# Kernel tuning notes

Measured on AMD Instinct MI355X. Metric: run time of the kernel, lower is better.

Reference implementation:

```python
import jax, jax.numpy as jnp
import numpy as np

N_NODES = 100000
N_EDGES = 800000
D_IN = 128
HOPS = 2
BN_EPS = 1e-5


def setup_inputs() -> dict:
    key = jax.random.key(0)
    ks = jax.random.split(key, 12)
    d_cat = D_IN * (HOPS + 1)  # 384
    inp = {
        "x": jax.random.normal(ks[0], (N_NODES, D_IN), dtype=jnp.float32),
        "edge_index": jax.random.randint(ks[1], (2, N_EDGES), 0, N_NODES, dtype=jnp.int32),
        "W0": jax.random.normal(ks[2], (HOPS + 1, D_IN, D_IN), dtype=jnp.float32) / np.sqrt(D_IN),
        "b0": jax.random.normal(ks[3], (HOPS + 1, D_IN), dtype=jnp.float32) * 0.01,
        "W1": jax.random.normal(ks[4], (HOPS + 1, d_cat, D_IN), dtype=jnp.float32) / np.sqrt(d_cat),
        "b1": jax.random.normal(ks[5], (HOPS + 1, D_IN), dtype=jnp.float32) * 0.01,
        "W2": jax.random.normal(ks[6], (HOPS + 1, d_cat, D_IN), dtype=jnp.float32) / np.sqrt(d_cat),
        "b2": jax.random.normal(ks[7], (HOPS + 1, D_IN), dtype=jnp.float32) * 0.01,
        "bn_gamma": jnp.ones((2, d_cat), dtype=jnp.float32),
        "bn_beta": jnp.zeros((2, d_cat), dtype=jnp.float32),
    }
    return inp


def _gcn_norm(edge_index, n):
    # gcn_norm(add_self_loops=False): deg over col, w_e = d^-1/2[row]*d^-1/2[col]
    row, col = edge_index[0], edge_index[1]
    deg = jax.ops.segment_sum(jnp.ones(row.shape[0], jnp.float32), col, num_segments=n)
    dinv = jnp.where(deg > 0, jax.lax.rsqrt(jnp.maximum(deg, 1.0)), 0.0)
    w = dinv[row] * dinv[col]
    return row, col, w


def _spmm(row, col, w, xj, n):
    # adj_t = SparseTensor(row=col, col=row, value=w): out[col_e] += w_e * x[row_e]
    return jax.ops.segment_sum(w[:, None] * xj[row], col, num_segments=n)


def _mixhop_layer(x, W, b, row, col, w, n):
    outs = [x @ W[0] + b[0]]
    for j in range(1, HOPS + 1):
        xj = x @ W[j] + b[j]
        for _ in range(j):
            xj = _spmm(row, col, w, xj, n)
        outs.append(xj)
    return jnp.concatenate(outs, axis=1)


def _bn(x, g, b):
    mu = jnp.mean(x, axis=0)
    var = jnp.mean(jnp.square(x - mu), axis=0)
    return (x - mu) * jax.lax.rsqrt(var + BN_EPS) * g + b


def reference(x, edge_index, W0, b0, W1, b1, W2, b2, bn_gamma, bn_beta):
    n = x.shape[0]
    row, col, w = _gcn_norm(edge_index, n)
    h = _mixhop_layer(x, W0, b0, row, col, w, n)
    h = jax.nn.relu(_bn(h, bn_gamma[0], bn_beta[0]))  # dropout: eval mode (identity)
    h = _mixhop_layer(h, W1, b1, row, col, w, n)
    h = jax.nn.relu(_bn(h, bn_gamma[1], bn_beta[1]))
    h = _mixhop_layer(h, W2, b2, row, col, w, n)
    return h
```

## Files before the change

kernel.cpp:

```cpp
#include <hip/hip_runtime.h>
#include <hip/hip_bf16.h>

#define NN 100000
#define NE 800000
#define DIN 128
#define DCAT 384
#define BN_EPS 1e-5

typedef __attribute__((ext_vector_type(8))) short bf16x8;
typedef __attribute__((ext_vector_type(4))) float f32x4;
typedef __attribute__((ext_vector_type(4))) int   i32x4;


__global__ void count_deg_k(const int* __restrict__ ei, int* __restrict__ deg) {
    int i = blockIdx.x * blockDim.x + threadIdx.x;
    if (i < NE) atomicAdd(&deg[ei[NE + i]], 1);
}

__global__ void dinv_k(const int* __restrict__ deg, float* __restrict__ dinv) {
    int i = blockIdx.x * blockDim.x + threadIdx.x;
    if (i < NN) {
        int d = deg[i];
        dinv[i] = (d > 0) ? rsqrtf((float)d) : 0.f;
    }
}

__global__ void scan1_k(const int* __restrict__ deg, int* __restrict__ out,
                        int* __restrict__ bsum) {
    __shared__ int s[1024];
    int i = blockIdx.x * 1024 + threadIdx.x;
    int v = (i < NN) ? deg[i] : 0;
    s[threadIdx.x] = v;
    __syncthreads();
    for (int off = 1; off < 1024; off <<= 1) {
        int t = (threadIdx.x >= off) ? s[threadIdx.x - off] : 0;
        __syncthreads();
        s[threadIdx.x] += t;
        __syncthreads();
    }
    if (i < NN) out[i] = s[threadIdx.x] - v;
    if (threadIdx.x == 1023) bsum[blockIdx.x] = s[1023];
}

__global__ void scan2_k(int* __restrict__ bsum, int nb) {
    if (threadIdx.x == 0) {
        int acc = 0;
        for (int b = 0; b < nb; ++b) { int v = bsum[b]; bsum[b] = acc; acc += v; }
    }
}

__global__ void scan3_k(int* __restrict__ ptr, int* __restrict__ cursor,
                        const int* __restrict__ bsum) {
    int i = blockIdx.x * 1024 + threadIdx.x;
    if (i < NN) {
        int p = ptr[i] + bsum[blockIdx.x];
        ptr[i] = p;
        cursor[i] = p;
    }
    if (i == NN) ptr[NN] = NE;
}

__global__ void scatter_k(const int* __restrict__ ei, const float* __restrict__ dinv,
                          int* __restrict__ cursor, int* __restrict__ crow,
                          float* __restrict__ cw) {
    int i = blockIdx.x * blockDim.x + threadIdx.x;
    if (i >= NE) return;
    int r = ei[i];
    int c = ei[NE + i];
    int p = atomicAdd(&cursor[c], 1);
    crow[p] = r;
    cw[p] = dinv[r] * dinv[c];
}


__device__ inline void split_trunc(float x, short& hi, short& lo) {
    unsigned u = __builtin_bit_cast(unsigned, x);
    hi = (short)(u >> 16);
    float hf = __builtin_bit_cast(float, u & 0xFFFF0000u);
    __hip_bfloat16 l = __float2bfloat16(x - hf);
    lo = *reinterpret_cast<short*>(&l);
}

__global__ void wsplit_k(const float* __restrict__ W, int K,
                         short* __restrict__ Wth, short* __restrict__ Wtl) {
    int i = blockIdx.x * 256 + threadIdx.x;
    if (i >= 3 * K * 128) return;
    int c = i & 127;
    int k = (i >> 7) % K;
    int j = i / (K * 128);
    short h, l;
    split_trunc(W[i], h, l);
    size_t o = (size_t)j * 128 * 384 + (size_t)c * 384 + k;
    Wth[o] = h;
    Wtl[o] = l;
}

__global__ __launch_bounds__(256) void bnsplit_k(
    const float* __restrict__ H, int Kc4,
    const float2* __restrict__ coef, int use_bn,
    short* __restrict__ Xh, short* __restrict__ Xl) {
    size_t n4 = (size_t)NN * Kc4;
    for (size_t i = (size_t)blockIdx.x * blockDim.x + threadIdx.x; i < n4;
         i += (size_t)gridDim.x * blockDim.x) {
        float4 v = ((const float4*)H)[i];
        if (use_bn) {
            int c4 = (int)(i % Kc4) * 4;
            float2 c0 = coef[c4 + 0], c1 = coef[c4 + 1];
            float2 c2 = coef[c4 + 2], c3 = coef[c4 + 3];
            v.x = fmaxf(v.x * c0.x + c0.y, 0.f);
            v.y = fmaxf(v.y * c1.x + c1.y, 0.f);
            v.z = fmaxf(v.z * c2.x + c2.y, 0.f);
            v.w = fmaxf(v.w * c3.x + c3.y, 0.f);
        }
        short h0, l0, h1, l1, h2, l2, h3, l3;
        split_trunc(v.x, h0, l0);
        split_trunc(v.y, h1, l1);
        split_trunc(v.z, h2, l2);
        split_trunc(v.w, h3, l3);
        ((short4*)Xh)[i] = make_short4(h0, h1, h2, h3);
        ((short4*)Xl)[i] = make_short4(l0, l1, l2, l3);
    }
}

#define GPITCH 40

__global__ __launch_bounds__(256, 3) void gemm3m_k(
    const short* __restrict__ Xh, const short* __restrict__ Xl, int K,
    const short* __restrict__ Wth, const short* __restrict__ Wtl,
    const float* __restrict__ bias,
    float* __restrict__ o0, int p0,
    float* __restrict__ o1, int p1,
    float* __restrict__ o2, int p2) {
    __shared__ short Ah[2][128 * GPITCH];
    __shared__ short Al[2][128 * GPITCH];

    const int nwg = gridDim.x;
    const int id  = blockIdx.x;
    const int q = nwg >> 3, r = nwg & 7;
    const int xcd = id & 7, ii = id >> 3;
    const int swz = (xcd < r ? xcd * (q + 1) : r * (q + 1) + (xcd - r) * q) + ii;
    const int j  = swz % 3;
    const int m0 = (swz / 3) * 128;

    const int t    = threadIdx.x;
    const int lane = t & 63;
    const int wv   = t >> 6;
    const int wr   = (wv >> 1) * 64;
    const int wc   = (wv & 1) * 64;
    const int lr   = lane & 15;
    const int lk   = lane >> 4;

    const short* Wh = Wth + (size_t)j * 128 * 384;
    const short* Wl = Wtl + (size_t)j * 128 * 384;

    const int arow = t >> 1;
    const int akc  = (t & 1) * 16;
    int gr = m0 + arow;
    if (gr >= NN) gr = NN - 1;
    const short* pAh = Xh + (size_t)gr * K + akc;
    const short* pAl = Xl + (size_t)gr * K + akc;
    const int soff = arow * GPITCH + akc;

    f32x4 acc[4][4];
#pragma unroll
    for (int a = 0; a < 4; ++a)
#pragma unroll
        for (int b = 0; b < 4; ++b) acc[a][b] = (f32x4){0.f, 0.f, 0.f, 0.f};

    const int NT = K >> 5;

    {
        i32x4 h0 = *(const i32x4*)(pAh);
        i32x4 h1 = *(const i32x4*)(pAh + 8);
        i32x4 l0 = *(const i32x4*)(pAl);
        i32x4 l1 = *(const i32x4*)(pAl + 8);
        *(i32x4*)&Ah[0][soff]     = h0;
        *(i32x4*)&Ah[0][soff + 8] = h1;
        *(i32x4*)&Al[0][soff]     = l0;
        *(i32x4*)&Al[0][soff + 8] = l1;
    }
    __syncthreads();

    int cur = 0;
    for (int tt = 0; tt < NT; ++tt) {
        const int kb = tt << 5;

        bf16x8 bh[4], bl[4];
#pragma unroll
        for (int nc = 0; nc < 4; ++nc) {
            const size_t bo = (size_t)(wc + nc * 16 + lr) * 384 + kb + lk * 8;
            bh[nc] = *(const bf16x8*)(Wh + bo);
            bl[nc] = *(const bf16x8*)(Wl + bo);
        }

        i32x4 h0, h1, l0, l1;
        if (tt + 1 < NT) {
            const int ko = kb + 32;
            h0 = *(const i32x4*)(pAh + ko);
            h1 = *(const i32x4*)(pAh + ko + 8);
            l0 = *(const i32x4*)(pAl + ko);
            l1 = *(const i32x4*)(pAl + ko + 8);
        }

        bf16x8 ah[4], al[4];
#pragma unroll
        for (int mr = 0; mr < 4; ++mr) {
            const int rr = (wr + mr * 16 + lr) * GPITCH + lk * 8;
            ah[mr] = *(const bf16x8*)&Ah[cur][rr];
            al[mr] = *(const bf16x8*)&Al[cur][rr];
        }

#pragma unroll
        for (int nc = 0; nc < 4; ++nc) {
#pragma unroll
            for (int mr = 0; mr < 4; ++mr) {
                f32x4 a = acc[mr][nc];
                a = __builtin_amdgcn_mfma_f32_16x16x32_bf16(al[mr], bh[nc], a, 0, 0, 0);
                a = __builtin_amdgcn_mfma_f32_16x16x32_bf16(ah[mr], bl[nc], a, 0, 0, 0);
                a = __builtin_amdgcn_mfma_f32_16x16x32_bf16(ah[mr], bh[nc], a, 0, 0, 0);
                acc[mr][nc] = a;
            }
        }

        if (tt + 1 < NT) {
            const int nb = cur ^ 1;
            *(i32x4*)&Ah[nb][soff]     = h0;
            *(i32x4*)&Ah[nb][soff + 8] = h1;
            *(i32x4*)&Al[nb][soff]     = l0;
            *(i32x4*)&Al[nb][soff + 8] = l1;
        }
        __syncthreads();
        cur ^= 1;
    }

    float* dst;
    int pitch;
    if (j == 0)      { dst = o0; pitch = p0; }
    else if (j == 1) { dst = o1; pitch = p1; }
    else             { dst = o2; pitch = p2; }

#pragma unroll
    for (int nc = 0; nc < 4; ++nc) {
        int col = wc + nc * 16 + lr;
        float bv = bias[j * 128 + col];
#pragma unroll
        for (int mr = 0; mr < 4; ++mr) {
            f32x4 a = acc[mr][nc];
#pragma unroll
            for (int rr = 0; rr < 4; ++rr) {
                int row = m0 + wr + mr * 16 + lk * 4 + rr;
                if (row < NN) dst[(size_t)row * pitch + col] = a[rr] + bv;
            }
        }
    }
}

__global__ __launch_bounds__(256) void spmm2_k(
    const int* __restrict__ ptr, const int* __restrict__ rows,
    const float* __restrict__ wv,
    const float* __restrict__ inAB,
    float* __restrict__ outA,
    float* __restrict__ outB) {
    int wid  = (blockIdx.x * blockDim.x + threadIdx.x) >> 6;
    int lane = threadIdx.x & 63;
    if (wid >= NN) return;
    int e0 = ptr[wid], e1 = ptr[wid + 1];
    float4 acc = make_float4(0.f, 0.f, 0.f, 0.f);
    int e = e0;
    for (; e + 2 <= e1; e += 2) {
        int   r0 = rows[e],  r1 = rows[e + 1];
        float w0 = wv[e],    w1 = wv[e + 1];
        float4 v0 = ((const float4*)(inAB + (size_t)r0 * 256))[lane];
        float4 v1 = ((const float4*)(inAB + (size_t)r1 * 256))[lane];
        acc.x += w0 * v0.x + w1 * v1.x;
        acc.y += w0 * v0.y + w1 * v1.y;
        acc.z += w0 * v0.z + w1 * v1.z;
        acc.w += w0 * v0.w + w1 * v1.w;
    }
    if (e < e1) {
        int   r0 = rows[e];
        float w0 = wv[e];
        float4 v0 = ((const float4*)(inAB + (size_t)r0 * 256))[lane];
        acc.x += w0 * v0.x;
        acc.y += w0 * v0.y;
        acc.z += w0 * v0.z;
        acc.w += w0 * v0.w;
    }
    if (lane < 32) ((float4*)(outA + (size_t)wid * 384))[lane] = acc;
    else           ((float4*)(outB + (size_t)wid * 128))[lane - 32] = acc;
}

__global__ __launch_bounds__(256) void spmm_k(
    const int* __restrict__ ptr, const int* __restrict__ rows,
    const float* __restrict__ wv,
    const float* __restrict__ xin,
    float* __restrict__ xout, int pout) {
    int wid  = (blockIdx.x * blockDim.x + threadIdx.x) >> 6;
    int lane = threadIdx.x & 63;
    if (wid >= NN) return;
    int e0 = ptr[wid], e1 = ptr[wid + 1];
    int half = lane >> 5;
    int cl   = lane & 31;
    float4 acc = make_float4(0.f, 0.f, 0.f, 0.f);
    int e = e0;
    for (; e + 4 <= e1; e += 4) {
        int   ra = rows[e + half],     rb = rows[e + 2 + half];
        float wa = wv[e + half],       wb = wv[e + 2 + half];
        float4 va = ((const float4*)(xin + (size_t)ra * 128))[cl];
        float4 vb = ((const float4*)(xin + (size_t)rb * 128))[cl];
        acc.x += wa * va.x + wb * vb.x;
        acc.y += wa * va.y + wb * vb.y;
        acc.z += wa * va.z + wb * vb.z;
        acc.w += wa * va.w + wb * vb.w;
    }
    for (; e + 2 <= e1; e += 2) {
        int   ra = rows[e + half];
        float wa = wv[e + half];
        float4 va = ((const float4*)(xin + (size_t)ra * 128))[cl];
        acc.x += wa * va.x;
        acc.y += wa * va.y;
        acc.z += wa * va.z;
        acc.w += wa * va.w;
    }
    if (e < e1 && half == 0) {
        int   ra = rows[e];
        float wa = wv[e];
        float4 va = ((const float4*)(xin + (size_t)ra * 128))[cl];
        acc.x += wa * va.x;
        acc.y += wa * va.y;
        acc.z += wa * va.z;
        acc.w += wa * va.w;
    }
    float4 o;
    o.x = acc.x + __shfl_xor(acc.x, 32);
    o.y = acc.y + __shfl_xor(acc.y, 32);
    o.z = acc.z + __shfl_xor(acc.z, 32);
    o.w = acc.w + __shfl_xor(acc.w, 32);
    if (half == 0) ((float4*)(xout + (size_t)wid * pout))[cl] = o;
}

#define BN_ROWS 256
#define BN_NBLK ((NN + BN_ROWS - 1) / BN_ROWS)

__global__ void bn_stats1_k(const float* __restrict__ H, float* __restrict__ partial) {
    int c  = threadIdx.x;
    int r0 = blockIdx.x * BN_ROWS;
    int r1 = min(r0 + BN_ROWS, NN);
    float s = 0.f, s2 = 0.f;
    for (int r = r0; r < r1; ++r) {
        float v = H[(size_t)r * DCAT + c];
        s  += v;
        s2 += v * v;
    }
    partial[blockIdx.x * 768 + c]       = s;
    partial[blockIdx.x * 768 + 384 + c] = s2;
}

__global__ void bn_finalize_k(const float* __restrict__ partial,
                              const float* __restrict__ g, const float* __restrict__ b,
                              float2* __restrict__ coef) {
    int c = threadIdx.x;
    double s = 0.0, s2 = 0.0;
    for (int i = 0; i < BN_NBLK; ++i) {
        s  += (double)partial[i * 768 + c];
        s2 += (double)partial[i * 768 + 384 + c];
    }
    double mu  = s / (double)NN;
    double var = s2 / (double)NN - mu * mu;
    double inv = 1.0 / sqrt(var + (double)BN_EPS);
    float scale = (float)((double)g[c] * inv);
    float shift = (float)((double)b[c] - mu * (double)g[c] * inv);
    coef[c] = make_float2(scale, shift);
}


static void run_layer(const short* Xh, const short* Xl, int K,
                      const float* W, const float* bias,
                      float* Hout, float* tmpAB, float* tmpC,
                      short* Wth, short* Wtl,
                      const int* ptr, const int* crow, const float* cw,
                      hipStream_t stream) {
    int nw = 3 * K * 128;
    wsplit_k<<<(nw + 255) / 256, 256, 0, stream>>>(W, K, Wth, Wtl);
    int nwg = 3 * ((NN + 127) / 128);
    gemm3m_k<<<nwg, 256, 0, stream>>>(Xh, Xl, K, Wth, Wtl, bias,
                                      Hout, DCAT, tmpAB, 256, tmpAB + 128, 256);
    int sg = (NN * 64 + 255) / 256;
    spmm2_k<<<sg, 256, 0, stream>>>(ptr, crow, cw, tmpAB, Hout + 128, tmpC);
    spmm_k<<<sg, 256, 0, stream>>>(ptr, crow, cw, tmpC, Hout + 256, DCAT);
}

extern "C" void kernel_launch(void* const* d_in, const int* in_sizes, int n_in,
                              void* d_out, int out_size, void* d_ws, size_t ws_size,
                              hipStream_t stream) {
    const float* x        = (const float*)d_in[0];
    const int*   ei       = (const int*)d_in[1];
    const float* W0       = (const float*)d_in[2];
    const float* b0       = (const float*)d_in[3];
    const float* W1       = (const float*)d_in[4];
    const float* b1       = (const float*)d_in[5];
    const float* W2       = (const float*)d_in[6];
    const float* b2       = (const float*)d_in[7];
    const float* bn_gamma = (const float*)d_in[8];
    const float* bn_beta  = (const float*)d_in[9];
    float* out = (float*)d_out;

    char* p = (char*)d_ws;
    auto alloc = [&](size_t bytes) -> void* {
        void* r = (void*)p;
        p += (bytes + 511) & ~(size_t)511;
        return r;
    };
    short* Xh      = (short*)alloc((size_t)NN * DCAT * 2);
    short* Xl      = (short*)alloc((size_t)NN * DCAT * 2);
    float* tmpAB   = (float*)alloc((size_t)NN * 256 * 4);
    float* Hws     = (float*)alloc((size_t)NN * DCAT * 4);
    int*   deg     = (int*)alloc((size_t)NN * 4);
    float* dinv    = (float*)alloc((size_t)NN * 4);
    int*   ptr     = (int*)alloc((size_t)(NN + 1) * 4);
    int*   cursor  = (int*)alloc((size_t)NN * 4);
    int*   bsum    = (int*)alloc(1024);
    int*   crow    = (int*)alloc((size_t)NE * 4);
    float* cw      = (float*)alloc((size_t)NE * 4);
    float* partial = (float*)alloc((size_t)BN_NBLK * 768 * 4);
    float2* coef   = (float2*)alloc(384 * 8);
    short* Wth     = (short*)alloc((size_t)3 * 128 * 384 * 2);
    short* Wtl     = (short*)alloc((size_t)3 * 128 * 384 * 2);
    float* tmpC = (float*)Xh;

    hipMemsetAsync(deg, 0, (size_t)NN * 4, stream);
    count_deg_k<<<(NE + 255) / 256, 256, 0, stream>>>(ei, deg);
    dinv_k<<<(NN + 255) / 256, 256, 0, stream>>>(deg, dinv);
    int nsb = (NN + 1023) / 1024;
    scan1_k<<<nsb, 1024, 0, stream>>>(deg, ptr, bsum);
    scan2_k<<<1, 64, 0, stream>>>(bsum, nsb);
    scan3_k<<<nsb, 1024, 0, stream>>>(ptr, cursor, bsum);
    scatter_k<<<(NE + 255) / 256, 256, 0, stream>>>(ei, dinv, cursor, crow, cw);

    bnsplit_k<<<2048, 256, 0, stream>>>(x, DIN / 4, coef, 0, Xh, Xl);
    run_layer(Xh, Xl, DIN, W0, b0, out, tmpAB, tmpC, Wth, Wtl, ptr, crow, cw, stream);
    bn_stats1_k<<<BN_NBLK, 384, 0, stream>>>(out, partial);
    bn_finalize_k<<<1, 384, 0, stream>>>(partial, bn_gamma, bn_beta, coef);

    bnsplit_k<<<2048, 256, 0, stream>>>(out, DCAT / 4, coef, 1, Xh, Xl);
    run_layer(Xh, Xl, DCAT, W1, b1, Hws, tmpAB, tmpC, Wth, Wtl, ptr, crow, cw, stream);
    bn_stats1_k<<<BN_NBLK, 384, 0, stream>>>(Hws, partial);
    bn_finalize_k<<<1, 384, 0, stream>>>(partial, bn_gamma + DCAT, bn_beta + DCAT, coef);

    bnsplit_k<<<2048, 256, 0, stream>>>(Hws, DCAT / 4, coef, 1, Xh, Xl);
    run_layer(Xh, Xl, DCAT, W2, b2, out, tmpAB, tmpC, Wth, Wtl, ptr, crow, cw, stream);
}
```

Before: 1.813 ms.

## Pack CSR edges as int2, stage W in LDS, unroll SpMM gathers deeper

Edge row index and weight are packed into one int2 array so each SpMM edge needs a single 8-byte load instead of two separate loads. The SpMM loops are unrolled to four gathers in flight per iteration to raise memory-level parallelism. The split-bf16 GEMM now stages W tiles through LDS alongside X, using a single buffer with two barriers per k-step instead of the double-buffered A path and direct global B loads. It also uses a plain 2D grid without XCD swizzling and raises the occupancy hint to 4. This trades GEMM load/compute overlap and L2 locality for less register pressure and more resident waves.

```diff
diff --git a/kernel.cpp b/kernel.cpp
--- a/kernel.cpp
+++ b/kernel.cpp
@@ -61,15 +61,14 @@
 }
 
 __global__ void scatter_k(const int* __restrict__ ei, const float* __restrict__ dinv,
-                          int* __restrict__ cursor, int* __restrict__ crow,
-                          float* __restrict__ cw) {
+                          int* __restrict__ cursor, int2* __restrict__ epack) {
     int i = blockIdx.x * blockDim.x + threadIdx.x;
     if (i >= NE) return;
     int r = ei[i];
     int c = ei[NE + i];
     int p = atomicAdd(&cursor[c], 1);
-    crow[p] = r;
-    cw[p] = dinv[r] * dinv[c];
+    float w = dinv[r] * dinv[c];
+    epack[p] = make_int2(r, __builtin_bit_cast(int, w));
 }
 
 
@@ -124,23 +123,20 @@
 
 #define GPITCH 40
 
-__global__ __launch_bounds__(256, 3) void gemm3m_k(
+__global__ __launch_bounds__(256, 4) void gemm3s_k(
     const short* __restrict__ Xh, const short* __restrict__ Xl, int K,
     const short* __restrict__ Wth, const short* __restrict__ Wtl,
     const float* __restrict__ bias,
     float* __restrict__ o0, int p0,
     float* __restrict__ o1, int p1,
     float* __restrict__ o2, int p2) {
-    __shared__ short Ah[2][128 * GPITCH];
-    __shared__ short Al[2][128 * GPITCH];
-
-    const int nwg = gridDim.x;
-    const int id  = blockIdx.x;
-    const int q = nwg >> 3, r = nwg & 7;
-    const int xcd = id & 7, ii = id >> 3;
-    const int swz = (xcd < r ? xcd * (q + 1) : r * (q + 1) + (xcd - r) * q) + ii;
-    const int j  = swz % 3;
-    const int m0 = (swz / 3) * 128;
+    __shared__ short Ah[128 * GPITCH];
+    __shared__ short Al[128 * GPITCH];
+    __shared__ short Bh[128 * GPITCH];
+    __shared__ short Bl[128 * GPITCH];
+
+    const int j  = blockIdx.y;
+    const int m0 = blockIdx.x * 128;
 
     const int t    = threadIdx.x;
     const int lane = t & 63;
@@ -153,13 +149,15 @@
     const short* Wh = Wth + (size_t)j * 128 * 384;
     const short* Wl = Wtl + (size_t)j * 128 * 384;
 
-    const int arow = t >> 1;
-    const int akc  = (t & 1) * 16;
-    int gr = m0 + arow;
+    const int srow = t >> 1;
+    const int skc  = (t & 1) * 16;
+    int gr = m0 + srow;
     if (gr >= NN) gr = NN - 1;
-    const short* pAh = Xh + (size_t)gr * K + akc;
-    const short* pAl = Xl + (size_t)gr * K + akc;
-    const int soff = arow * GPITCH + akc;
+    const short* pAh = Xh + (size_t)gr * K + skc;
+    const short* pAl = Xl + (size_t)gr * K + skc;
+    const short* pBh = Wh + (size_t)srow * 384 + skc;
+    const short* pBl = Wl + (size_t)srow * 384 + skc;
+    const int soff = srow * GPITCH + skc;
 
     f32x4 acc[4][4];
 #pragma unroll
@@ -167,70 +165,48 @@
 #pragma unroll
         for (int b = 0; b < 4; ++b) acc[a][b] = (f32x4){0.f, 0.f, 0.f, 0.f};
 
-    const int NT = K >> 5;
-
-    {
-        i32x4 h0 = *(const i32x4*)(pAh);
-        i32x4 h1 = *(const i32x4*)(pAh + 8);
-        i32x4 l0 = *(const i32x4*)(pAl);
-        i32x4 l1 = *(const i32x4*)(pAl + 8);
-        *(i32x4*)&Ah[0][soff]     = h0;
-        *(i32x4*)&Ah[0][soff + 8] = h1;
-        *(i32x4*)&Al[0][soff]     = l0;
-        *(i32x4*)&Al[0][soff + 8] = l1;
-    }
-    __syncthreads();
-
-    int cur = 0;
-    for (int tt = 0; tt < NT; ++tt) {
-        const int kb = tt << 5;
-
-        bf16x8 bh[4], bl[4];
-#pragma unroll
-        for (int nc = 0; nc < 4; ++nc) {
-            const size_t bo = (size_t)(wc + nc * 16 + lr) * 384 + kb + lk * 8;
-            bh[nc] = *(const bf16x8*)(Wh + bo);
-            bl[nc] = *(const bf16x8*)(Wl + bo);
-        }
-
-        i32x4 h0, h1, l0, l1;
-        if (tt + 1 < NT) {
-            const int ko = kb + 32;
-            h0 = *(const i32x4*)(pAh + ko);
-            h1 = *(const i32x4*)(pAh + ko + 8);
-            l0 = *(const i32x4*)(pAl + ko);
-            l1 = *(const i32x4*)(pAl + ko + 8);
-        }
+    for (int kb = 0; kb < K; kb += 32) {
+        i32x4 a0 = *(const i32x4*)(pAh + kb);
+        i32x4 a1 = *(const i32x4*)(pAh + kb + 8);
+        i32x4 a2 = *(const i32x4*)(pAl + kb);
+        i32x4 a3 = *(const i32x4*)(pAl + kb + 8);
+        i32x4 b0 = *(const i32x4*)(pBh + kb);
+        i32x4 b1 = *(const i32x4*)(pBh + kb + 8);
+        i32x4 b2 = *(const i32x4*)(pBl + kb);
+        i32x4 b3 = *(const i32x4*)(pBl + kb + 8);
+
+        __syncthreads();
+        *(i32x4*)&Ah[soff]     = a0;
+        *(i32x4*)&Ah[soff + 8] = a1;
+        *(i32x4*)&Al[soff]     = a2;
+        *(i32x4*)&Al[soff + 8] = a3;
+        *(i32x4*)&Bh[soff]     = b0;
+        *(i32x4*)&Bh[soff + 8] = b1;
+        *(i32x4*)&Bl[soff]     = b2;
+        *(i32x4*)&Bl[soff + 8] = b3;
+        __syncthreads();
 
         bf16x8 ah[4], al[4];
 #pragma unroll
         for (int mr = 0; mr < 4; ++mr) {
             const int rr = (wr + mr * 16 + lr) * GPITCH + lk * 8;
-            ah[mr] = *(const bf16x8*)&Ah[cur][rr];
-            al[mr] = *(const bf16x8*)&Al[cur][rr];
+            ah[mr] = *(const bf16x8*)&Ah[rr];
+            al[mr] = *(const bf16x8*)&Al[rr];
         }
-
 #pragma unroll
         for (int nc = 0; nc < 4; ++nc) {
+            const int cc = (wc + nc * 16 + lr) * GPITCH + lk * 8;
+            bf16x8 bh = *(const bf16x8*)&Bh[cc];
+            bf16x8 bl = *(const bf16x8*)&Bl[cc];
 #pragma unroll
             for (int mr = 0; mr < 4; ++mr) {
                 f32x4 a = acc[mr][nc];
-                a = __builtin_amdgcn_mfma_f32_16x16x32_bf16(al[mr], bh[nc], a, 0, 0, 0);
-                a = __builtin_amdgcn_mfma_f32_16x16x32_bf16(ah[mr], bl[nc], a, 0, 0, 0);
-                a = __builtin_amdgcn_mfma_f32_16x16x32_bf16(ah[mr], bh[nc], a, 0, 0, 0);
+                a = __builtin_amdgcn_mfma_f32_16x16x32_bf16(al[mr], bh, a, 0, 0, 0);
+                a = __builtin_amdgcn_mfma_f32_16x16x32_bf16(ah[mr], bl, a, 0, 0, 0);
+                a = __builtin_amdgcn_mfma_f32_16x16x32_bf16(ah[mr], bh, a, 0, 0, 0);
                 acc[mr][nc] = a;
             }
         }
-
-        if (tt + 1 < NT) {
-            const int nb = cur ^ 1;
-            *(i32x4*)&Ah[nb][soff]     = h0;
-            *(i32x4*)&Ah[nb][soff + 8] = h1;
-            *(i32x4*)&Al[nb][soff]     = l0;
-            *(i32x4*)&Al[nb][soff + 8] = l1;
-        }
-        __syncthreads();
-        cur ^= 1;
     }
 
     float* dst;
@@ -256,8 +232,7 @@
 }
 
 __global__ __launch_bounds__(256) void spmm2_k(
-    const int* __restrict__ ptr, const int* __restrict__ rows,
-    const float* __restrict__ wv,
+    const int* __restrict__ ptr, const int2* __restrict__ ep,
     const float* __restrict__ inAB,
     float* __restrict__ outA,
     float* __restrict__ outB) {
@@ -267,20 +242,25 @@
     int e0 = ptr[wid], e1 = ptr[wid + 1];
     float4 acc = make_float4(0.f, 0.f, 0.f, 0.f);
     int e = e0;
-    for (; e + 2 <= e1; e += 2) {
-        int   r0 = rows[e],  r1 = rows[e + 1];
-        float w0 = wv[e],    w1 = wv[e + 1];
-        float4 v0 = ((const float4*)(inAB + (size_t)r0 * 256))[lane];
-        float4 v1 = ((const float4*)(inAB + (size_t)r1 * 256))[lane];
-        acc.x += w0 * v0.x + w1 * v1.x;
-        acc.y += w0 * v0.y + w1 * v1.y;
-        acc.z += w0 * v0.z + w1 * v1.z;
-        acc.w += w0 * v0.w + w1 * v1.w;
-    }
-    if (e < e1) {
-        int   r0 = rows[e];
-        float w0 = wv[e];
-        float4 v0 = ((const float4*)(inAB + (size_t)r0 * 256))[lane];
+    for (; e + 4 <= e1; e += 4) {
+        int2 q0 = ep[e], q1 = ep[e + 1], q2 = ep[e + 2], q3 = ep[e + 3];
+        float4 v0 = ((const float4*)(inAB + (size_t)q0.x * 256))[lane];
+        float4 v1 = ((const float4*)(inAB + (size_t)q1.x * 256))[lane];
+        float4 v2 = ((const float4*)(inAB + (size_t)q2.x * 256))[lane];
+        float4 v3 = ((const float4*)(inAB + (size_t)q3.x * 256))[lane];
+        float w0 = __builtin_bit_cast(float, q0.y);
+        float w1 = __builtin_bit_cast(float, q1.y);
+        float w2 = __builtin_bit_cast(float, q2.y);
+        float w3 = __builtin_bit_cast(float, q3.y);
+        acc.x += w0 * v0.x + w1 * v1.x + w2 * v2.x + w3 * v3.x;
+        acc.y += w0 * v0.y + w1 * v1.y + w2 * v2.y + w3 * v3.y;
+        acc.z += w0 * v0.z + w1 * v1.z + w2 * v2.z + w3 * v3.z;
+        acc.w += w0 * v0.w + w1 * v1.w + w2 * v2.w + w3 * v3.w;
+    }
+    for (; e < e1; ++e) {
+        int2 q0 = ep[e];
+        float w0 = __builtin_bit_cast(float, q0.y);
+        float4 v0 = ((const float4*)(inAB + (size_t)q0.x * 256))[lane];
         acc.x += w0 * v0.x;
         acc.y += w0 * v0.y;
         acc.z += w0 * v0.z;
@@ -291,8 +271,7 @@
 }
 
 __global__ __launch_bounds__(256) void spmm_k(
-    const int* __restrict__ ptr, const int* __restrict__ rows,
-    const float* __restrict__ wv,
+    const int* __restrict__ ptr, const int2* __restrict__ ep,
     const float* __restrict__ xin,
     float* __restrict__ xout, int pout) {
     int wid  = (blockIdx.x * blockDim.x + threadIdx.x) >> 6;
@@ -303,33 +282,39 @@
     int cl   = lane & 31;
     float4 acc = make_float4(0.f, 0.f, 0.f, 0.f);
     int e = e0;
-    for (; e + 4 <= e1; e += 4) {
-        int   ra = rows[e + half],     rb = rows[e + 2 + half];
-        float wa = wv[e + half],       wb = wv[e + 2 + half];
-        float4 va = ((const float4*)(xin + (size_t)ra * 128))[cl];
-        float4 vb = ((const float4*)(xin + (size_t)rb * 128))[cl];
-        acc.x += wa * va.x + wb * vb.x;
-        acc.y += wa * va.y + wb * vb.y;
-        acc.z += wa * va.z + wb * vb.z;
-        acc.w += wa * va.w + wb * vb.w;
+    for (; e + 8 <= e1; e += 8) {
+        int2 q0 = ep[e + half],     q1 = ep[e + 2 + half];
+        int2 q2 = ep[e + 4 + half], q3 = ep[e + 6 + half];
+        float4 v0 = ((const float4*)(xin + (size_t)q0.x * 128))[cl];
+        float4 v1 = ((const float4*)(xin + (size_t)q1.x * 128))[cl];
+        float4 v2 = ((const float4*)(xin + (size_t)q2.x * 128))[cl];
+        float4 v3 = ((const float4*)(xin + (size_t)q3.x * 128))[cl];
+        float w0 = __builtin_bit_cast(float, q0.y);
+        float w1 = __builtin_bit_cast(float, q1.y);
+        float w2 = __builtin_bit_cast(float, q2.y);
+        float w3 = __builtin_bit_cast(float, q3.y);
+        acc.x += w0 * v0.x + w1 * v1.x + w2 * v2.x + w3 * v3.x;
+        acc.y += w0 * v0.y + w1 * v1.y + w2 * v2.y + w3 * v3.y;
+        acc.z += w0 * v0.z + w1 * v1.z + w2 * v2.z + w3 * v3.z;
+        acc.w += w0 * v0.w + w1 * v1.w + w2 * v2.w + w3 * v3.w;
     }
     for (; e + 2 <= e1; e += 2) {
-        int   ra = rows[e + half];
-        float wa = wv[e + half];
-        float4 va = ((const float4*)(xin + (size_t)ra * 128))[cl];
-        acc.x += wa * va.x;
-        acc.y += wa * va.y;
-        acc.z += wa * va.z;
-        acc.w += wa * va.w;
+        int2 q0 = ep[e + half];
+        float w0 = __builtin_bit_cast(float, q0.y);
+        float4 v0 = ((const float4*)(xin + (size_t)q0.x * 128))[cl];
+        acc.x += w0 * v0.x;
+        acc.y += w0 * v0.y;
+        acc.z += w0 * v0.z;
+        acc.w += w0 * v0.w;
     }
     if (e < e1 && half == 0) {
-        int   ra = rows[e];
-        float wa = wv[e];
-        float4 va = ((const float4*)(xin + (size_t)ra * 128))[cl];
-        acc.x += wa * va.x;
-        acc.y += wa * va.y;
-        acc.z += wa * va.z;
-        acc.w += wa * va.w;
+        int2 q0 = ep[e];
+        float w0 = __builtin_bit_cast(float, q0.y);
+        float4 v0 = ((const float4*)(xin + (size_t)q0.x * 128))[cl];
+        acc.x += w0 * v0.x;
+        acc.y += w0 * v0.y;
+        acc.z += w0 * v0.z;
+        acc.w += w0 * v0.w;
     }
     float4 o;
     o.x = acc.x + __shfl_xor(acc.x, 32);
@@ -378,16 +363,16 @@
                       const float* W, const float* bias,
                       float* Hout, float* tmpAB, float* tmpC,
                       short* Wth, short* Wtl,
-                      const int* ptr, const int* crow, const float* cw,
+                      const int* ptr, const int2* ep,
                       hipStream_t stream) {
     int nw = 3 * K * 128;
     wsplit_k<<<(nw + 255) / 256, 256, 0, stream>>>(W, K, Wth, Wtl);
-    int nwg = 3 * ((NN + 127) / 128);
-    gemm3m_k<<<nwg, 256, 0, stream>>>(Xh, Xl, K, Wth, Wtl, bias,
-                                      Hout, DCAT, tmpAB, 256, tmpAB + 128, 256);
+    dim3 g((NN + 127) / 128, 3);
+    gemm3s_k<<<g, 256, 0, stream>>>(Xh, Xl, K, Wth, Wtl, bias,
+                                    Hout, DCAT, tmpAB, 256, tmpAB + 128, 256);
     int sg = (NN * 64 + 255) / 256;
-    spmm2_k<<<sg, 256, 0, stream>>>(ptr, crow, cw, tmpAB, Hout + 128, tmpC);
-    spmm_k<<<sg, 256, 0, stream>>>(ptr, crow, cw, tmpC, Hout + 256, DCAT);
+    spmm2_k<<<sg, 256, 0, stream>>>(ptr, ep, tmpAB, Hout + 128, tmpC);
+    spmm_k<<<sg, 256, 0, stream>>>(ptr, ep, tmpC, Hout + 256, DCAT);
 }
 
 extern "C" void kernel_launch(void* const* d_in, const int* in_sizes, int n_in,
@@ -420,8 +405,7 @@
     int*   ptr     = (int*)alloc((size_t)(NN + 1) * 4);
     int*   cursor  = (int*)alloc((size_t)NN * 4);
     int*   bsum    = (int*)alloc(1024);
-    int*   crow    = (int*)alloc((size_t)NE * 4);
-    float* cw      = (float*)alloc((size_t)NE * 4);
+    int2*  epack   = (int2*)alloc((size_t)NE * 8);
     float* partial = (float*)alloc((size_t)BN_NBLK * 768 * 4);
     float2* coef   = (float2*)alloc(384 * 8);
     short* Wth     = (short*)alloc((size_t)3 * 128 * 384 * 2);
@@ -435,18 +419,18 @@
     scan1_k<<<nsb, 1024, 0, stream>>>(deg, ptr, bsum);
     scan2_k<<<1, 64, 0, stream>>>(bsum, nsb);
     scan3_k<<<nsb, 1024, 0, stream>>>(ptr, cursor, bsum);
-    scatter_k<<<(NE + 255) / 256, 256, 0, stream>>>(ei, dinv, cursor, crow, cw);
+    scatter_k<<<(NE + 255) / 256, 256, 0, stream>>>(ei, dinv, cursor, epack);
 
     bnsplit_k<<<2048, 256, 0, stream>>>(x, DIN / 4, coef, 0, Xh, Xl);
-    run_layer(Xh, Xl, DIN, W0, b0, out, tmpAB, tmpC, Wth, Wtl, ptr, crow, cw, stream);
+    run_layer(Xh, Xl, DIN, W0, b0, out, tmpAB, tmpC, Wth, Wtl, ptr, epack, stream);
     bn_stats1_k<<<BN_NBLK, 384, 0, stream>>>(out, partial);
     bn_finalize_k<<<1, 384, 0, stream>>>(partial, bn_gamma, bn_beta, coef);
 
     bnsplit_k<<<2048, 256, 0, stream>>>(out, DCAT / 4, coef, 1, Xh, Xl);
-    run_layer(Xh, Xl, DCAT, W1, b1, Hws, tmpAB, tmpC, Wth, Wtl, ptr, crow, cw, stream);
+    run_layer(Xh, Xl, DCAT, W1, b1, Hws, tmpAB, tmpC, Wth, Wtl, ptr, epack, stream);
     bn_stats1_k<<<BN_NBLK, 384, 0, stream>>>(Hws, partial);
     bn_finalize_k<<<1, 384, 0, stream>>>(partial, bn_gamma + DCAT, bn_beta + DCAT, coef);
 
     bnsplit_k<<<2048, 256, 0, stream>>>(Hws, DCAT / 4, coef, 1, Xh, Xl);
-    run_layer(Xh, Xl, DCAT, W2, b2, out, tmpAB, tmpC, Wth, Wtl, ptr, crow, cw, stream);
-}
+    run_layer(Xh, Xl, DCAT, W2, b2, out, tmpAB, tmpC, Wth, Wtl, ptr, epack, stream);
+}
```

Measured after the change: 1.682 ms. 1.08x faster.
